# Performance work log

Measured on AMD Instinct MI355X. Metric: run time of the kernel, lower is better.

Reference implementation:

```python
import jax, jax.numpy as jnp
import numpy as np

EMBED_DIM = 1024
NUM_HEADS = 16
HEAD_DIM = EMBED_DIM // NUM_HEADS  # 64
GROUP_SIZE = 4                     # 4 values packed per uint8 (2-bit KIVI)
Q_LEVELS = 3.0                     # 2-bit -> codes in [0, 3]
Q_HALF = 1.5                       # symmetric offset


def kivi_fake_quant(k):
    """Per-group 2-bit quantize+dequantize of keys, KIVI-style.
    k: [B, H, S, D] float32. Groups of GROUP_SIZE along D share one fp32 scale
    (mirrors k_cache_packed uint8 codes + k_scales fp32 in the source).
    """
    B, H, S, D = k.shape
    g = k.reshape(B, H, S, D // GROUP_SIZE, GROUP_SIZE)
    max_abs = jnp.max(jnp.abs(g), axis=-1, keepdims=True)        # per-group scale basis
    scale = max_abs / Q_HALF
    safe = jnp.where(scale == 0, 1.0, scale)
    codes = jnp.clip(jnp.round(g / safe + Q_HALF), 0.0, Q_LEVELS)  # uint8 codes (as float)
    deq = (codes - Q_HALF) * scale                                 # dequant
    return deq.reshape(B, H, S, D)


def split_heads(x):
    B, S, E = x.shape
    return x.reshape(B, S, NUM_HEADS, HEAD_DIM).transpose(0, 2, 1, 3)  # [B,H,S,d]


def setup_inputs() -> dict:
    key = jax.random.key(0)
    k1, k2, k3 = jax.random.split(key, 3)
    B, S = 4, 1024
    return {
        "hidden_states": jax.random.normal(k1, (B, S, EMBED_DIM), jnp.float32),
        "attention_mask": jnp.zeros((B, S), jnp.float32),  # additive mask
        "w_attn": jax.random.normal(k2, (EMBED_DIM, 3 * EMBED_DIM), jnp.float32) * 0.02,
        "b_attn": jnp.zeros((3 * EMBED_DIM,), jnp.float32),
        "w_proj": jax.random.normal(k3, (EMBED_DIM, EMBED_DIM), jnp.float32) * 0.02,
        "b_proj": jnp.zeros((EMBED_DIM,), jnp.float32),
    }


def reference(hidden_states, attention_mask, w_attn, b_attn, w_proj, b_proj):
    B, S, E = hidden_states.shape
    qkv = hidden_states @ w_attn + b_attn            # GPT-2 Conv1D: x @ W + b
    q, k, v = jnp.split(qkv, 3, axis=2)
    q, k, v = split_heads(q), split_heads(k), split_heads(v)   # [B,H,S,d]

    k_deq = kivi_fake_quant(k)                       # quantized KV cache (keys)
    # kivi_sycl.batched_attention: q @ dequant(K)^T over full cache_len (== S here)
    scores = jnp.einsum('bhqd,bhkd->bhqk', q, k_deq)
    # source adds 2-D additive mask BEFORE the 1/sqrt(d) scaling
    scores = scores + attention_mask[:, None, None, :]
    attn = jax.nn.softmax(scores / jnp.sqrt(jnp.float32(HEAD_DIM)), axis=-1)

    out = jnp.einsum('bhqk,bhkd->bhqd', attn, v)     # V cache kept fp32
    out = out.transpose(0, 2, 1, 3).reshape(B, S, E)
    return out @ w_proj + b_proj
```

## Files before the change

kernel.cpp:

```cpp
#include <hip/hip_runtime.h>
#include <math.h>

#define S_LEN 1024
#define B_SZ  4
#define E_DIM 1024
#define NH    16
#define HD    64
#define GK    1024

typedef unsigned short u16;
typedef _Float16 f16;
typedef __attribute__((ext_vector_type(8))) _Float16 f16x8;
typedef __attribute__((ext_vector_type(2))) __fp16   hf16x2;
typedef __attribute__((ext_vector_type(4))) float    f32x4;

#define MFMA16(a, b, c) __builtin_amdgcn_mfma_f32_16x16x32_f16(a, b, c, 0, 0, 0)
#define SCALE2 0.18033688011112042f

__device__ __forceinline__ u16 f2h_bits(float f) {
    union { f16 h; u16 u; } c; c.h = (f16)f;
    return c.u;
}
__device__ __forceinline__ unsigned pk2h(float a, float b) {
    return (unsigned)f2h_bits(a) | ((unsigned)f2h_bits(b) << 16);
}
__device__ __forceinline__ unsigned pkrtz2(float a, float b) {
    hf16x2 t = __builtin_amdgcn_cvt_pkrtz(a, b);
    union { hf16x2 v; unsigned u; } c; c.v = t; return c.u;
}

__device__ __forceinline__ void glds16(const u16* g, u16* l) {
    __builtin_amdgcn_global_load_lds(
        (const __attribute__((address_space(1))) unsigned int*)g,
        (__attribute__((address_space(3))) unsigned int*)l, 16, 0, 0);
}

__global__ __launch_bounds__(256) void prep_all(
    const float* __restrict__ hs, u16* __restrict__ Hh,
    const float* __restrict__ w_attn, u16* __restrict__ Wqt,
    const float* __restrict__ w_proj, u16* __restrict__ Wpt,
    const float* __restrict__ mask, float* __restrict__ Msc)
{
    __shared__ float t[32][33];
    const int bid = blockIdx.x;

    if (bid == 8192) {
        const int i = threadIdx.x * 16;
        #pragma unroll
        for (int k = 0; k < 4; ++k) {
            float4 v = *(const float4*)&mask[i + 4 * k];
            float4 o = { v.x * SCALE2, v.y * SCALE2, v.z * SCALE2, v.w * SCALE2 };
            *(float4*)&Msc[i + 4 * k] = o;
        }
        return;
    }
    if (bid < 4096) {
        const size_t i = ((size_t)bid * 256 + threadIdx.x) * 4;
        float4 v = *(const float4*)&hs[i];
        ushort4 h;
        h.x = f2h_bits(v.x); h.y = f2h_bits(v.y);
        h.z = f2h_bits(v.z); h.w = f2h_bits(v.w);
        *(ushort4*)&Hh[i] = h;
        return;
    }

    const bool isA = bid < 7168;
    const int tt = isA ? (bid - 4096) : (bid - 7168);
    const int bxx = isA ? (tt % 96) : (tt % 32);
    const int byy = isA ? (tt / 96) : (tt / 32);
    const int N   = isA ? 3072 : 1024;
    const float* W = isA ? w_attn : w_proj;
    u16* Wt = isA ? Wqt : Wpt;

    const int k0 = byy * 32, n0 = bxx * 32;
    {
        const int kr = threadIdx.x >> 3, nc = (threadIdx.x & 7) << 2;
        float4 v = *(const float4*)&W[(size_t)(k0 + kr) * N + n0 + nc];
        t[kr][nc] = v.x; t[kr][nc + 1] = v.y; t[kr][nc + 2] = v.z; t[kr][nc + 3] = v.w;
    }
    __syncthreads();
    const int nr = threadIdx.x >> 3, kc = (threadIdx.x & 7) << 2;
    ushort4 h;
    h.x = f2h_bits(t[kc + 0][nr]); h.y = f2h_bits(t[kc + 1][nr]);
    h.z = f2h_bits(t[kc + 2][nr]); h.w = f2h_bits(t[kc + 3][nr]);
    *(ushort4*)&Wt[(size_t)(n0 + nr) * GK + k0 + kc] = h;
}

__global__ __launch_bounds__(256, 4) void qkv_gemm(
    const u16* __restrict__ A, const u16* __restrict__ Bt,
    const float* __restrict__ bias, u16* __restrict__ Qh,
    u16* __restrict__ Kh, u16* __restrict__ Vtg)
{
    __shared__ u16 SLDS[16896];
    u16* Asp = SLDS;
    u16* Bsp = SLDS + 8192;

    const int tid = threadIdx.x;
    const int wave = tid >> 6, lane = tid & 63;
    const int quad = lane >> 4, l15 = lane & 15;
    const int wr = wave >> 1, wc = wave & 1;

    const int m0   = blockIdx.y * 128;
    const int nloc = blockIdx.x * 128;
    const int region = nloc >> 10;

    const u16* Ab = A  + (size_t)m0 * GK;
    const u16* Bb = Bt + (size_t)nloc * GK;

    const int soff = (((lane & 7) ^ ((lane >> 3) & 7)) << 3);
    const int srow8 = lane >> 3;
    const int sw = l15 & 7;

    f32x4 acc[4][4] = {};

    for (int k0 = 0; k0 < GK; k0 += 64) {
        __syncthreads();
        #pragma unroll
        for (int i = 0; i < 4; ++i) {
            const int tI = wave * 4 + i;
            const int row = tI * 8 + srow8;
            glds16(Ab + (size_t)row * GK + k0 + soff, &Asp[tI * 512]);
            glds16(Bb + (size_t)row * GK + k0 + soff, &Bsp[tI * 512]);
        }
        __syncthreads();
        #pragma unroll
        for (int h = 0; h < 2; ++h) {
            const int cs = ((4 * h + quad) ^ sw) << 3;
            f16x8 af[4], bf[4];
            #pragma unroll
            for (int i = 0; i < 4; ++i)
                af[i] = *(const f16x8*)&Asp[(64 * wr + 16 * i + l15) * 64 + cs];
            #pragma unroll
            for (int j = 0; j < 4; ++j)
                bf[j] = *(const f16x8*)&Bsp[(64 * wc + 16 * j + l15) * 64 + cs];
            #pragma unroll
            for (int i = 0; i < 4; ++i)
                #pragma unroll
                for (int j = 0; j < 4; ++j)
                    acc[i][j] = MFMA16(af[i], bf[j], acc[i][j]);
        }
    }

    if (region == 2) {
        #pragma unroll
        for (int j = 0; j < 4; ++j) {
            const int colg = nloc + 64 * wc + 16 * j + l15;
            const float bv = bias[colg];
            const int cr = colg & 1023, h = cr >> 6, d = cr & 63;
            #pragma unroll
            for (int i = 0; i < 4; ++i) {
                const int rowb = m0 + 64 * wr + 16 * i + quad * 4;
                const int b = rowb >> 10, s0 = rowb & 1023;
                float v0 = acc[i][j][0] + bv, v1 = acc[i][j][1] + bv;
                float v2 = acc[i][j][2] + bv, v3 = acc[i][j][3] + bv;
                uint2 st = { pk2h(v0, v1), pk2h(v2, v3) };
                *(uint2*)&Vtg[((size_t)(b * NH + h) * HD + d) * S_LEN + s0] = st;
            }
        }
    } else {
        float* EP = (float*)SLDS;
        u16* dstg = (region == 1) ? Kh : Qh;
        #pragma unroll
        for (int p = 0; p < 2; ++p) {
            __syncthreads();
            if (wr == p) {
                #pragma unroll
                for (int i = 0; i < 4; ++i)
                    #pragma unroll
                    for (int j = 0; j < 4; ++j) {
                        const int colb = 64 * wc + 16 * j + l15;
                        const float bv = bias[nloc + colb];
                        #pragma unroll
                        for (int r = 0; r < 4; ++r)
                            EP[(16 * i + quad * 4 + r) * 132 + colb] = acc[i][j][r] + bv;
                    }
            }
            __syncthreads();
            const int rr = tid >> 2, cc = (tid & 3) * 32;
            const int rowg = m0 + 64 * p + rr;
            const int bb = rowg >> 10, ss = rowg & 1023;
            float v[32];
            #pragma unroll
            for (int k = 0; k < 8; ++k) {
                f32x4 t4 = *(const f32x4*)&EP[rr * 132 + cc + 4 * k];
                v[4 * k + 0] = t4[0]; v[4 * k + 1] = t4[1];
                v[4 * k + 2] = t4[2]; v[4 * k + 3] = t4[3];
            }
            if (region == 1) {
                #pragma unroll
                for (int g = 0; g < 8; ++g) {
                    float a = fmaxf(fmaxf(fabsf(v[4 * g]), fabsf(v[4 * g + 1])),
                                    fmaxf(fabsf(v[4 * g + 2]), fabsf(v[4 * g + 3])));
                    float scale = a * (1.0f / 1.5f);
                    float safe  = (scale == 0.0f) ? 1.0f : scale;
                    #pragma unroll
                    for (int r = 0; r < 4; ++r) {
                        float q = fminf(fmaxf(rintf(v[4 * g + r] / safe + 1.5f), 0.0f), 3.0f);
                        v[4 * g + r] = (q - 1.5f) * scale;
                    }
                }
            }
            unsigned w[16];
            #pragma unroll
            for (int m = 0; m < 16; ++m) w[m] = pk2h(v[2 * m], v[2 * m + 1]);
            const int hh = ((nloc & 1023) + cc) >> 6;
            const int d0 = cc & 63;
            u16* dp = dstg + (((size_t)(bb * NH + hh)) * S_LEN + ss) * HD + d0;
            #pragma unroll
            for (int q4 = 0; q4 < 4; ++q4) {
                uint4 st = { w[4 * q4], w[4 * q4 + 1], w[4 * q4 + 2], w[4 * q4 + 3] };
                *(uint4*)&dp[q4 * 8] = st;
            }
        }
    }
}

__global__ __launch_bounds__(256, 4) void proj_gemm(
    const u16* __restrict__ A, const u16* __restrict__ Bt,
    const float* __restrict__ bias, float* __restrict__ C)
{
    __shared__ u16 Asp[64 * 64];
    __shared__ u16 Bsp[64 * 64];

    const int tid = threadIdx.x;
    const int wave = tid >> 6, lane = tid & 63;
    const int quad = lane >> 4, l15 = lane & 15;
    const int wr = wave >> 1, wc = wave & 1;

    const int m0   = blockIdx.y * 64;
    const int nloc = blockIdx.x * 64;

    const u16* Ab = A  + (size_t)m0 * GK;
    const u16* Bb = Bt + (size_t)nloc * GK;

    const int soff = (((lane & 7) ^ ((lane >> 3) & 7)) << 3);
    const int srow8 = lane >> 3;
    const int sw = l15 & 7;

    f32x4 acc[2][2] = {};

    for (int k0 = 0; k0 < GK; k0 += 64) {
        __syncthreads();
        #pragma unroll
        for (int i = 0; i < 2; ++i) {
            const int tI = wave * 2 + i;
            glds16(Ab + (size_t)(tI * 8 + srow8) * GK + k0 + soff, &Asp[tI * 512]);
            glds16(Bb + (size_t)(tI * 8 + srow8) * GK + k0 + soff, &Bsp[tI * 512]);
        }
        __syncthreads();
        #pragma unroll
        for (int h = 0; h < 2; ++h) {
            const int cs = ((4 * h + quad) ^ sw) << 3;
            f16x8 af[2], bf[2];
            #pragma unroll
            for (int i = 0; i < 2; ++i)
                af[i] = *(const f16x8*)&Asp[(32 * wr + 16 * i + l15) * 64 + cs];
            #pragma unroll
            for (int j = 0; j < 2; ++j)
                bf[j] = *(const f16x8*)&Bsp[(32 * wc + 16 * j + l15) * 64 + cs];
            #pragma unroll
            for (int i = 0; i < 2; ++i)
                #pragma unroll
                for (int j = 0; j < 2; ++j)
                    acc[i][j] = MFMA16(af[i], bf[j], acc[i][j]);
        }
    }

    #pragma unroll
    for (int j = 0; j < 2; ++j) {
        const int col = nloc + 32 * wc + 16 * j + l15;
        const float bv = bias[col];
        #pragma unroll
        for (int i = 0; i < 2; ++i) {
            const int row = m0 + 32 * wr + 16 * i + quad * 4;
            #pragma unroll
            for (int r = 0; r < 4; ++r)
                C[(size_t)(row + r) * E_DIM + col] = acc[i][j][r] + bv;
        }
    }
}

__global__ __launch_bounds__(512, 4) void attn_mfma(
    const u16* __restrict__ Qh, const u16* __restrict__ Kh,
    const u16* __restrict__ Vtg, const float* __restrict__ Msc,
    u16* __restrict__ out)
{
    __shared__ u16 Ks[2][64 * 64];
    __shared__ u16 Vt[2][64 * 64];
    __shared__ u16 Ps[8][16 * 72];
    __shared__ float MsL[1024];

    const int tid  = threadIdx.x;
    const int wave = tid >> 6, lane = tid & 63;
    const int quad = lane >> 4, l15 = lane & 15;

    const int d = blockIdx.x;
    const int j = d >> 3;
    const int head = (d & 7) * 8 + (j & 7);
    const int qt   = j >> 3;
    const int b = head >> 4, h = head & 15;
    const size_t head_base = (size_t)head * (S_LEN * HD);

    if (tid < 256) {
        float4 mv = *(const float4*)&Msc[b * S_LEN + tid * 4];
        *(float4*)&MsL[tid * 4] = mv;
    }

    const int qbase = qt * 128 + wave * 16;
    f16x8 qf0, qf1;
    {
        const u16* qp = Qh + head_base + (size_t)(qbase + l15) * HD + quad * 8;
        qf0 = *(const f16x8*)qp;
        qf1 = *(const f16x8*)(qp + 32);
    }

    f32x4 O[4] = {};
    f32x4 ps_acc = {0.f, 0.f, 0.f, 0.f};

    const u16* Kb = Kh  + head_base;
    const u16* Vb = Vtg + head_base;

    const int srow_ = wave * 8 + (lane >> 3);
    const int skoff = (((lane & 7) ^ ((lane >> 3) & 7)) << 3);
    const int ch0 = ((quad ^ (l15 & 7)) << 3);
    const int ch1 = (((4 + quad) ^ (l15 & 7)) << 3);

    glds16(Kb + (size_t)srow_ * HD + skoff,    &Ks[0][wave * 512]);
    glds16(Vb + (size_t)srow_ * S_LEN + skoff, &Vt[0][wave * 512]);
    __syncthreads();

    for (int kt = 0; kt < 16; ++kt) {
        const int cur = kt & 1;

        if (kt < 15) {
            glds16(Kb + (size_t)((kt + 1) * 64 + srow_) * HD + skoff,
                   &Ks[cur ^ 1][wave * 512]);
            glds16(Vb + (size_t)srow_ * S_LEN + (kt + 1) * 64 + skoff,
                   &Vt[cur ^ 1][wave * 512]);
        }

        const u16* Kl = Ks[cur];
        const u16* Vl = Vt[cur];

        f32x4 acc[4] = {};
        __builtin_amdgcn_s_setprio(1);
        #pragma unroll
        for (int i = 0; i < 4; ++i) {
            const u16* kr = &Kl[(16 * i + l15) * 64];
            acc[i] = MFMA16(*(const f16x8*)&kr[ch0], qf0, acc[i]);
            acc[i] = MFMA16(*(const f16x8*)&kr[ch1], qf1, acc[i]);
        }
        __builtin_amdgcn_s_setprio(0);

        const float* mrow = &MsL[kt * 64];
        f32x4 p4[4];
        #pragma unroll
        for (int i = 0; i < 4; ++i) {
            f32x4 mk = *(const f32x4*)(mrow + 16 * i + quad * 4);
            f32x4 s = acc[i] * SCALE2 + mk;
            p4[i][0] = __builtin_amdgcn_exp2f(s[0]);
            p4[i][1] = __builtin_amdgcn_exp2f(s[1]);
            p4[i][2] = __builtin_amdgcn_exp2f(s[2]);
            p4[i][3] = __builtin_amdgcn_exp2f(s[3]);
            ps_acc += p4[i];
        }

        {
            u16* pw = &Ps[wave][l15 * 72];
            #pragma unroll
            for (int i = 0; i < 4; ++i) {
                *(unsigned*)&pw[16 * i + quad * 4]     = pkrtz2(p4[i][0], p4[i][1]);
                *(unsigned*)&pw[16 * i + quad * 4 + 2] = pkrtz2(p4[i][2], p4[i][3]);
            }
        }

        __builtin_amdgcn_s_setprio(1);
        #pragma unroll
        for (int kc = 0; kc < 2; ++kc) {
            f16x8 pa = *(const f16x8*)&Ps[wave][l15 * 72 + kc * 32 + quad * 8];
            const int chv = kc ? ch1 : ch0;
            #pragma unroll
            for (int i = 0; i < 4; ++i)
                O[i] = MFMA16(pa, *(const f16x8*)&Vl[(16 * i + l15) * 64 + chv], O[i]);
        }
        __builtin_amdgcn_s_setprio(0);

        __syncthreads();
    }

    float psum = (ps_acc[0] + ps_acc[1]) + (ps_acc[2] + ps_acc[3]);
    psum += __shfl_xor(psum, 16);
    psum += __shfl_xor(psum, 32);
    float li[4];
    #pragma unroll
    for (int r = 0; r < 4; ++r) li[r] = 1.0f / __shfl(psum, quad * 4 + r);
    #pragma unroll
    for (int r = 0; r < 4; ++r) {
        u16* orow = out + ((size_t)(b * S_LEN) + qbase + quad * 4 + r) * E_DIM
                    + h * HD + l15;
        orow[0]  = f2h_bits(O[0][r] * li[r]);
        orow[16] = f2h_bits(O[1][r] * li[r]);
        orow[32] = f2h_bits(O[2][r] * li[r]);
        orow[48] = f2h_bits(O[3][r] * li[r]);
    }
}

extern "C" void kernel_launch(void* const* d_in, const int* in_sizes, int n_in,
                              void* d_out, int out_size, void* d_ws, size_t ws_size,
                              hipStream_t stream)
{
    const float* hs     = (const float*)d_in[0];
    const float* mask   = (const float*)d_in[1];
    const float* w_attn = (const float*)d_in[2];
    const float* b_attn = (const float*)d_in[3];
    const float* w_proj = (const float*)d_in[4];
    const float* b_proj = (const float*)d_in[5];
    float* out = (float*)d_out;

    const size_t M1 = (size_t)4096 * 1024;
    u16* Ah   = (u16*)d_ws;
    u16* Wqt  = Ah   + M1;
    u16* Wpt  = Wqt  + 3 * M1;
    u16* Qh   = Wpt  + M1;
    u16* Kh   = Qh   + M1;
    u16* Vtg  = Kh   + M1;
    u16* AOh  = Vtg  + M1;
    float* Msc = (float*)(AOh + M1);

    prep_all<<<8193, 256, 0, stream>>>(hs, Ah, w_attn, Wqt, w_proj, Wpt, mask, Msc);

    qkv_gemm<<<dim3(24, 32), 256, 0, stream>>>(Ah, Wqt, b_attn, Qh, Kh, Vtg);

    attn_mfma<<<B_SZ * NH * (S_LEN / 128), 512, 0, stream>>>(Qh, Kh, Vtg, Msc, AOh);

    proj_gemm<<<dim3(16, 64), 256, 0, stream>>>(AOh, Wpt, b_proj, out);
}
```

Before: 168.5 us.

## Split attention key range across two wave groups per block with LDS merge

Each block now handles 64 query rows instead of 128, with two groups of four waves each covering half the key sequence (split-K). The partial outputs and row sums are merged through shared memory at the end, and the grid doubles to 1024 blocks. Double buffering is replaced by per-group single buffers with two syncs per tile, and the mask is read straight from global memory instead of being staged in LDS. The aim is more blocks and higher occupancy (launch bounds raised to 8), traded against lost load/compute overlap, twice as many Q and K/V loads per query, and the extra merge step.

```diff
diff --git a/kernel.cpp b/kernel.cpp
--- a/kernel.cpp
+++ b/kernel.cpp
@@ -280,33 +280,28 @@
     }
 }
 
-__global__ __launch_bounds__(512, 4) void attn_mfma(
+__global__ __launch_bounds__(512, 8) void attn_mfma(
     const u16* __restrict__ Qh, const u16* __restrict__ Kh,
     const u16* __restrict__ Vtg, const float* __restrict__ Msc,
     u16* __restrict__ out)
 {
     __shared__ u16 Ks[2][64 * 64];
     __shared__ u16 Vt[2][64 * 64];
-    __shared__ u16 Ps[8][16 * 72];
-    __shared__ float MsL[1024];
+    __shared__ u16 Ps[8][16 * 32];
 
     const int tid  = threadIdx.x;
     const int wave = tid >> 6, lane = tid & 63;
     const int quad = lane >> 4, l15 = lane & 15;
+    const int gw = wave & 3;
+    const int g  = wave >> 2;
 
     const int d = blockIdx.x;
-    const int j = d >> 3;
-    const int head = (d & 7) * 8 + (j & 7);
-    const int qt   = j >> 3;
+    const int head = (d & 7) * 8 + ((d >> 3) & 7);
+    const int qt   = d >> 6;
     const int b = head >> 4, h = head & 15;
     const size_t head_base = (size_t)head * (S_LEN * HD);
 
-    if (tid < 256) {
-        float4 mv = *(const float4*)&Msc[b * S_LEN + tid * 4];
-        *(float4*)&MsL[tid * 4] = mv;
-    }
-
-    const int qbase = qt * 128 + wave * 16;
+    const int qbase = qt * 64 + gw * 16;
     f16x8 qf0, qf1;
     {
         const u16* qp = Qh + head_base + (size_t)(qbase + l15) * HD + quad * 8;
@@ -320,75 +315,91 @@
     const u16* Kb = Kh  + head_base;
     const u16* Vb = Vtg + head_base;
 
-    const int srow_ = wave * 8 + (lane >> 3);
+    const int srow  = gw * 16 + (lane >> 3);
     const int skoff = (((lane & 7) ^ ((lane >> 3) & 7)) << 3);
     const int ch0 = ((quad ^ (l15 & 7)) << 3);
     const int ch1 = (((4 + quad) ^ (l15 & 7)) << 3);
 
-    glds16(Kb + (size_t)srow_ * HD + skoff,    &Ks[0][wave * 512]);
-    glds16(Vb + (size_t)srow_ * S_LEN + skoff, &Vt[0][wave * 512]);
-    __syncthreads();
-
-    for (int kt = 0; kt < 16; ++kt) {
-        const int cur = kt & 1;
-
-        if (kt < 15) {
-            glds16(Kb + (size_t)((kt + 1) * 64 + srow_) * HD + skoff,
-                   &Ks[cur ^ 1][wave * 512]);
-            glds16(Vb + (size_t)srow_ * S_LEN + (kt + 1) * 64 + skoff,
-                   &Vt[cur ^ 1][wave * 512]);
-        }
-
-        const u16* Kl = Ks[cur];
-        const u16* Vl = Vt[cur];
+    u16* KsG = Ks[g];
+    u16* VtG = Vt[g];
+    const float* mbase = Msc + b * S_LEN + g * 512;
+
+    for (int t = 0; t < 8; ++t) {
+        const int kt = g * 8 + t;
+        __syncthreads();
+        #pragma unroll
+        for (int p = 0; p < 2; ++p) {
+            glds16(Kb + (size_t)(kt * 64 + srow + p * 8) * HD + skoff,
+                   &KsG[(gw * 16 + p * 8) * 64]);
+            glds16(Vb + (size_t)(srow + p * 8) * S_LEN + kt * 64 + skoff,
+                   &VtG[(gw * 16 + p * 8) * 64]);
+        }
+        __syncthreads();
 
         f32x4 acc[4] = {};
         __builtin_amdgcn_s_setprio(1);
         #pragma unroll
         for (int i = 0; i < 4; ++i) {
-            const u16* kr = &Kl[(16 * i + l15) * 64];
+            const u16* kr = &KsG[(16 * i + l15) * 64];
             acc[i] = MFMA16(*(const f16x8*)&kr[ch0], qf0, acc[i]);
             acc[i] = MFMA16(*(const f16x8*)&kr[ch1], qf1, acc[i]);
         }
         __builtin_amdgcn_s_setprio(0);
 
-        const float* mrow = &MsL[kt * 64];
-        f32x4 p4[4];
+        const float* mrow = mbase + t * 64;
         #pragma unroll
         for (int i = 0; i < 4; ++i) {
             f32x4 mk = *(const f32x4*)(mrow + 16 * i + quad * 4);
             f32x4 s = acc[i] * SCALE2 + mk;
-            p4[i][0] = __builtin_amdgcn_exp2f(s[0]);
-            p4[i][1] = __builtin_amdgcn_exp2f(s[1]);
-            p4[i][2] = __builtin_amdgcn_exp2f(s[2]);
-            p4[i][3] = __builtin_amdgcn_exp2f(s[3]);
-            ps_acc += p4[i];
-        }
-
-        {
-            u16* pw = &Ps[wave][l15 * 72];
-            #pragma unroll
-            for (int i = 0; i < 4; ++i) {
-                *(unsigned*)&pw[16 * i + quad * 4]     = pkrtz2(p4[i][0], p4[i][1]);
-                *(unsigned*)&pw[16 * i + quad * 4 + 2] = pkrtz2(p4[i][2], p4[i][3]);
-            }
-        }
-
+            acc[i][0] = __builtin_amdgcn_exp2f(s[0]);
+            acc[i][1] = __builtin_amdgcn_exp2f(s[1]);
+            acc[i][2] = __builtin_amdgcn_exp2f(s[2]);
+            acc[i][3] = __builtin_amdgcn_exp2f(s[3]);
+            ps_acc += acc[i];
+        }
+
+        u16* pw = &Ps[wave][l15 * 32];
         __builtin_amdgcn_s_setprio(1);
         #pragma unroll
         for (int kc = 0; kc < 2; ++kc) {
-            f16x8 pa = *(const f16x8*)&Ps[wave][l15 * 72 + kc * 32 + quad * 8];
+            #pragma unroll
+            for (int ii = 0; ii < 2; ++ii) {
+                const int i = 2 * kc + ii;
+                *(unsigned*)&pw[16 * ii + quad * 4]     = pkrtz2(acc[i][0], acc[i][1]);
+                *(unsigned*)&pw[16 * ii + quad * 4 + 2] = pkrtz2(acc[i][2], acc[i][3]);
+            }
+            f16x8 pa = *(const f16x8*)&pw[quad * 8];
             const int chv = kc ? ch1 : ch0;
             #pragma unroll
             for (int i = 0; i < 4; ++i)
-                O[i] = MFMA16(pa, *(const f16x8*)&Vl[(16 * i + l15) * 64 + chv], O[i]);
+                O[i] = MFMA16(pa, *(const f16x8*)&VtG[(16 * i + l15) * 64 + chv], O[i]);
         }
         __builtin_amdgcn_s_setprio(0);
-
-        __syncthreads();
-    }
+    }
+
+    __syncthreads();
+    float* SC = (float*)Ks;
+    if (g == 1) {
+        float* p = SC + (gw * 64 + lane) * 21;
+        #pragma unroll
+        for (int i = 0; i < 4; ++i)
+            #pragma unroll
+            for (int r = 0; r < 4; ++r) p[4 * i + r] = O[i][r];
+        p[16] = (ps_acc[0] + ps_acc[1]) + (ps_acc[2] + ps_acc[3]);
+    }
+    __syncthreads();
+    if (g == 1) return;
 
     float psum = (ps_acc[0] + ps_acc[1]) + (ps_acc[2] + ps_acc[3]);
+    {
+        const float* p = SC + (gw * 64 + lane) * 21;
+        #pragma unroll
+        for (int i = 0; i < 4; ++i)
+            #pragma unroll
+            for (int r = 0; r < 4; ++r) O[i][r] += p[4 * i + r];
+        psum += p[16];
+    }
+
     psum += __shfl_xor(psum, 16);
     psum += __shfl_xor(psum, 32);
     float li[4];
@@ -431,7 +442,7 @@
 
     qkv_gemm<<<dim3(24, 32), 256, 0, stream>>>(Ah, Wqt, b_attn, Qh, Kh, Vtg);
 
-    attn_mfma<<<B_SZ * NH * (S_LEN / 128), 512, 0, stream>>>(Qh, Kh, Vtg, Msc, AOh);
+    attn_mfma<<<1024, 512, 0, stream>>>(Qh, Kh, Vtg, Msc, AOh);
 
     proj_gemm<<<dim3(16, 64), 256, 0, stream>>>(AOh, Wpt, b_proj, out);
 }
```

New measurement: 203.1 us. +20.5%, slower.

## Double-buffer QKV GEMM LDS tiles with K=32 steps and MFMA priority boost

Applied to the files above, without the earlier changes.

The QKV GEMM main loop now uses two LDS buffers with a K-step of 32 instead of a single 64-wide buffer. The next tile's global-to-LDS loads are issued before the current tile's MFMAs, and only one barrier remains per iteration. The swizzle is reworked for the 32-wide rows, and s_setprio is raised around the MFMA block. This is meant to overlap memory latency with compute, at the cost of twice as many loop iterations and barriers over K.

```diff
diff --git a/kernel.cpp b/kernel.cpp
--- a/kernel.cpp
+++ b/kernel.cpp
@@ -92,8 +92,6 @@
     u16* __restrict__ Kh, u16* __restrict__ Vtg)
 {
     __shared__ u16 SLDS[16896];
-    u16* Asp = SLDS;
-    u16* Bsp = SLDS + 8192;
 
     const int tid = threadIdx.x;
     const int wave = tid >> 6, lane = tid & 63;
@@ -107,38 +105,54 @@
     const u16* Ab = A  + (size_t)m0 * GK;
     const u16* Bb = Bt + (size_t)nloc * GK;
 
-    const int soff = (((lane & 7) ^ ((lane >> 3) & 7)) << 3);
-    const int srow8 = lane >> 3;
-    const int sw = l15 & 7;
+    const int r16 = lane >> 2;
+    const int sg  = (((lane & 3) ^ ((r16 >> 1) & 3)) << 3);
+    const int rk  = ((quad ^ ((l15 >> 1) & 3)) << 3);
 
     f32x4 acc[4][4] = {};
 
-    for (int k0 = 0; k0 < GK; k0 += 64) {
+    #pragma unroll
+    for (int i = 0; i < 2; ++i) {
+        const int tI = wave * 2 + i;
+        glds16(Ab + (size_t)(tI * 16 + r16) * GK + sg,        SLDS + tI * 512);
+        glds16(Bb + (size_t)(tI * 16 + r16) * GK + sg, SLDS + 8192 + tI * 512);
+    }
+    __syncthreads();
+
+    for (int kt = 0; kt < 32; ++kt) {
+        const int cur = kt & 1;
+        u16* As = SLDS + cur * 4096;
+        u16* Bs = SLDS + 8192 + cur * 4096;
+
+        if (kt < 31) {
+            u16* An = SLDS + (cur ^ 1) * 4096;
+            u16* Bn = SLDS + 8192 + (cur ^ 1) * 4096;
+            const int k1 = (kt + 1) * 32;
+            #pragma unroll
+            for (int i = 0; i < 2; ++i) {
+                const int tI = wave * 2 + i;
+                glds16(Ab + (size_t)(tI * 16 + r16) * GK + k1 + sg, An + tI * 512);
+                glds16(Bb + (size_t)(tI * 16 + r16) * GK + k1 + sg, Bn + tI * 512);
+            }
+        }
+
+        f16x8 af[4], bf[4];
+        #pragma unroll
+        for (int i = 0; i < 4; ++i)
+            af[i] = *(const f16x8*)&As[(64 * wr + 16 * i + l15) * 32 + rk];
+        #pragma unroll
+        for (int j = 0; j < 4; ++j)
+            bf[j] = *(const f16x8*)&Bs[(64 * wc + 16 * j + l15) * 32 + rk];
+
+        __builtin_amdgcn_s_setprio(1);
+        #pragma unroll
+        for (int i = 0; i < 4; ++i)
+            #pragma unroll
+            for (int j = 0; j < 4; ++j)
+                acc[i][j] = MFMA16(af[i], bf[j], acc[i][j]);
+        __builtin_amdgcn_s_setprio(0);
+
         __syncthreads();
-        #pragma unroll
-        for (int i = 0; i < 4; ++i) {
-            const int tI = wave * 4 + i;
-            const int row = tI * 8 + srow8;
-            glds16(Ab + (size_t)row * GK + k0 + soff, &Asp[tI * 512]);
-            glds16(Bb + (size_t)row * GK + k0 + soff, &Bsp[tI * 512]);
-        }
-        __syncthreads();
-        #pragma unroll
-        for (int h = 0; h < 2; ++h) {
-            const int cs = ((4 * h + quad) ^ sw) << 3;
-            f16x8 af[4], bf[4];
-            #pragma unroll
-            for (int i = 0; i < 4; ++i)
-                af[i] = *(const f16x8*)&Asp[(64 * wr + 16 * i + l15) * 64 + cs];
-            #pragma unroll
-            for (int j = 0; j < 4; ++j)
-                bf[j] = *(const f16x8*)&Bsp[(64 * wc + 16 * j + l15) * 64 + cs];
-            #pragma unroll
-            for (int i = 0; i < 4; ++i)
-                #pragma unroll
-                for (int j = 0; j < 4; ++j)
-                    acc[i][j] = MFMA16(af[i], bf[j], acc[i][j]);
-        }
     }
 
     if (region == 2) {
```

New measurement: 167.4 us. Within noise of the previous version (-0.6%).

## Enlarge QKV GEMM tiles to 256x256 with double-buffered LDS prefetch

Applied to the files above, without the earlier changes.

The QKV GEMM moves from 128x128 tiles with 256 threads to 256x256 tiles with 512 threads, a double-buffered LDS pipeline that prefetches the next K-slice while computing the current one, and raised wave priority around the MFMA bursts. The epilogue is restructured into chunked passes through a shared staging buffer so the K quantization and Q/K/V layout writes still fit. This aims to raise arithmetic intensity and overlap global loads with MFMA work. In exchange the grid shrinks to 192 blocks, which may underfill the 256 CUs, and register and LDS use per block grows.

```diff
diff --git a/kernel.cpp b/kernel.cpp
--- a/kernel.cpp
+++ b/kernel.cpp
@@ -86,59 +86,73 @@
     *(ushort4*)&Wt[(size_t)(n0 + nr) * GK + k0 + kc] = h;
 }
 
-__global__ __launch_bounds__(256, 4) void qkv_gemm(
+__global__ __launch_bounds__(512, 2) void qkv_gemm(
     const u16* __restrict__ A, const u16* __restrict__ Bt,
     const float* __restrict__ bias, u16* __restrict__ Qh,
     u16* __restrict__ Kh, u16* __restrict__ Vtg)
 {
-    __shared__ u16 SLDS[16896];
-    u16* Asp = SLDS;
-    u16* Bsp = SLDS + 8192;
+    __shared__ u16 SLDS[65536];
 
     const int tid = threadIdx.x;
     const int wave = tid >> 6, lane = tid & 63;
     const int quad = lane >> 4, l15 = lane & 15;
-    const int wr = wave >> 1, wc = wave & 1;
-
-    const int m0   = blockIdx.y * 128;
-    const int nloc = blockIdx.x * 128;
+    const int wr = wave >> 2, wc = wave & 3;
+
+    const int m0   = blockIdx.y * 256;
+    const int nloc = blockIdx.x * 256;
     const int region = nloc >> 10;
 
     const u16* Ab = A  + (size_t)m0 * GK;
     const u16* Bb = Bt + (size_t)nloc * GK;
 
-    const int soff = (((lane & 7) ^ ((lane >> 3) & 7)) << 3);
     const int srow8 = lane >> 3;
-    const int sw = l15 & 7;
-
-    f32x4 acc[4][4] = {};
-
-    for (int k0 = 0; k0 < GK; k0 += 64) {
-        __syncthreads();
-        #pragma unroll
-        for (int i = 0; i < 4; ++i) {
-            const int tI = wave * 4 + i;
-            const int row = tI * 8 + srow8;
-            glds16(Ab + (size_t)row * GK + k0 + soff, &Asp[tI * 512]);
-            glds16(Bb + (size_t)row * GK + k0 + soff, &Bsp[tI * 512]);
-        }
-        __syncthreads();
-        #pragma unroll
-        for (int h = 0; h < 2; ++h) {
-            const int cs = ((4 * h + quad) ^ sw) << 3;
-            f16x8 af[4], bf[4];
-            #pragma unroll
-            for (int i = 0; i < 4; ++i)
-                af[i] = *(const f16x8*)&Asp[(64 * wr + 16 * i + l15) * 64 + cs];
+    const int soff  = (((lane & 7) ^ (srow8 & 7)) << 3);
+    const int sw    = l15 & 7;
+
+    f32x4 acc[8][4] = {};
+
+    auto STAGE = [&](int kt, int bsel) {
+        u16* Ad = SLDS + bsel * 16384;
+        u16* Bd = SLDS + 32768 + bsel * 16384;
+        const int k0 = kt * 64;
+        #pragma unroll
+        for (int r = 0; r < 4; ++r) {
+            const int g = wave * 4 + r;
+            const int row = g * 8 + srow8;
+            glds16(Ab + (size_t)row * GK + k0 + soff, Ad + g * 512);
+            glds16(Bb + (size_t)row * GK + k0 + soff, Bd + g * 512);
+        }
+    };
+
+    STAGE(0, 0);
+    __syncthreads();
+
+    for (int kt = 0; kt < 16; ++kt) {
+        const int cur = kt & 1;
+        if (kt < 15) STAGE(kt + 1, cur ^ 1);
+
+        const u16* As = SLDS + cur * 16384;
+        const u16* Bs = SLDS + 32768 + cur * 16384;
+
+        #pragma unroll
+        for (int kh = 0; kh < 2; ++kh) {
+            const int cs = ((4 * kh + quad) ^ sw) << 3;
+            f16x8 af[8], bf[4];
+            #pragma unroll
+            for (int i = 0; i < 8; ++i)
+                af[i] = *(const f16x8*)&As[(128 * wr + 16 * i + l15) * 64 + cs];
             #pragma unroll
             for (int j = 0; j < 4; ++j)
-                bf[j] = *(const f16x8*)&Bsp[(64 * wc + 16 * j + l15) * 64 + cs];
-            #pragma unroll
-            for (int i = 0; i < 4; ++i)
+                bf[j] = *(const f16x8*)&Bs[(64 * wc + 16 * j + l15) * 64 + cs];
+            __builtin_amdgcn_s_setprio(1);
+            #pragma unroll
+            for (int i = 0; i < 8; ++i)
                 #pragma unroll
                 for (int j = 0; j < 4; ++j)
                     acc[i][j] = MFMA16(af[i], bf[j], acc[i][j]);
-        }
+            __builtin_amdgcn_s_setprio(0);
+        }
+        __syncthreads();
     }
 
     if (region == 2) {
@@ -148,8 +162,8 @@
             const float bv = bias[colg];
             const int cr = colg & 1023, h = cr >> 6, d = cr & 63;
             #pragma unroll
-            for (int i = 0; i < 4; ++i) {
-                const int rowb = m0 + 64 * wr + 16 * i + quad * 4;
+            for (int i = 0; i < 8; ++i) {
+                const int rowb = m0 + 128 * wr + 16 * i + quad * 4;
                 const int b = rowb >> 10, s0 = rowb & 1023;
                 float v0 = acc[i][j][0] + bv, v1 = acc[i][j][1] + bv;
                 float v2 = acc[i][j][2] + bv, v3 = acc[i][j][3] + bv;
@@ -160,56 +174,67 @@
     } else {
         float* EP = (float*)SLDS;
         u16* dstg = (region == 1) ? Kh : Qh;
-        #pragma unroll
-        for (int p = 0; p < 2; ++p) {
-            __syncthreads();
-            if (wr == p) {
-                #pragma unroll
-                for (int i = 0; i < 4; ++i)
+        for (int p = 0; p < 4; ++p) {
+            for (int ch = 0; ch < 2; ++ch) {
+                __syncthreads();
+                if (wr == (p >> 1) && (wc >> 1) == ch) {
+                    const int wcl = wc & 1;
                     #pragma unroll
-                    for (int j = 0; j < 4; ++j) {
-                        const int colb = 64 * wc + 16 * j + l15;
-                        const float bv = bias[nloc + colb];
+                    for (int ii = 0; ii < 4; ++ii) {
+                        const int i = 4 * (p & 1) + ii;
                         #pragma unroll
-                        for (int r = 0; r < 4; ++r)
-                            EP[(16 * i + quad * 4 + r) * 132 + colb] = acc[i][j][r] + bv;
-                    }
-            }
-            __syncthreads();
-            const int rr = tid >> 2, cc = (tid & 3) * 32;
-            const int rowg = m0 + 64 * p + rr;
-            const int bb = rowg >> 10, ss = rowg & 1023;
-            float v[32];
-            #pragma unroll
-            for (int k = 0; k < 8; ++k) {
-                f32x4 t4 = *(const f32x4*)&EP[rr * 132 + cc + 4 * k];
-                v[4 * k + 0] = t4[0]; v[4 * k + 1] = t4[1];
-                v[4 * k + 2] = t4[2]; v[4 * k + 3] = t4[3];
-            }
-            if (region == 1) {
-                #pragma unroll
-                for (int g = 0; g < 8; ++g) {
-                    float a = fmaxf(fmaxf(fabsf(v[4 * g]), fabsf(v[4 * g + 1])),
-                                    fmaxf(fabsf(v[4 * g + 2]), fabsf(v[4 * g + 3])));
-                    float scale = a * (1.0f / 1.5f);
-                    float safe  = (scale == 0.0f) ? 1.0f : scale;
-                    #pragma unroll
-                    for (int r = 0; r < 4; ++r) {
-                        float q = fminf(fmaxf(rintf(v[4 * g + r] / safe + 1.5f), 0.0f), 3.0f);
-                        v[4 * g + r] = (q - 1.5f) * scale;
+                        for (int j = 0; j < 4; ++j) {
+                            const int colb = 64 * wcl + 16 * j + l15;
+                            const float bv = bias[nloc + 128 * ch + colb];
+                            #pragma unroll
+                            for (int r = 0; r < 4; ++r)
+                                EP[(16 * ii + quad * 4 + r) * 132 + colb] =
+                                    acc[i][j][r] + bv;
+                        }
                     }
                 }
-            }
-            unsigned w[16];
-            #pragma unroll
-            for (int m = 0; m < 16; ++m) w[m] = pk2h(v[2 * m], v[2 * m + 1]);
-            const int hh = ((nloc & 1023) + cc) >> 6;
-            const int d0 = cc & 63;
-            u16* dp = dstg + (((size_t)(bb * NH + hh)) * S_LEN + ss) * HD + d0;
-            #pragma unroll
-            for (int q4 = 0; q4 < 4; ++q4) {
-                uint4 st = { w[4 * q4], w[4 * q4 + 1], w[4 * q4 + 2], w[4 * q4 + 3] };
-                *(uint4*)&dp[q4 * 8] = st;
+                __syncthreads();
+                if (tid < 256) {
+                    const int rr = tid >> 2, cc = (tid & 3) * 32;
+                    const int rowg = m0 + 64 * p + rr;
+                    const int bb = rowg >> 10, ss = rowg & 1023;
+                    float v[32];
+                    #pragma unroll
+                    for (int k = 0; k < 8; ++k) {
+                        f32x4 t4 = *(const f32x4*)&EP[rr * 132 + cc + 4 * k];
+                        v[4 * k + 0] = t4[0]; v[4 * k + 1] = t4[1];
+                        v[4 * k + 2] = t4[2]; v[4 * k + 3] = t4[3];
+                    }
+                    if (region == 1) {
+                        #pragma unroll
+                        for (int g = 0; g < 8; ++g) {
+                            float a = fmaxf(
+                                fmaxf(fabsf(v[4 * g]), fabsf(v[4 * g + 1])),
+                                fmaxf(fabsf(v[4 * g + 2]), fabsf(v[4 * g + 3])));
+                            float scale = a * (1.0f / 1.5f);
+                            float safe  = (scale == 0.0f) ? 1.0f : scale;
+                            #pragma unroll
+                            for (int r = 0; r < 4; ++r) {
+                                float q = fminf(fmaxf(
+                                    rintf(v[4 * g + r] / safe + 1.5f), 0.0f), 3.0f);
+                                v[4 * g + r] = (q - 1.5f) * scale;
+                            }
+                        }
+                    }
+                    unsigned w[16];
+                    #pragma unroll
+                    for (int m = 0; m < 16; ++m)
+                        w[m] = pk2h(v[2 * m], v[2 * m + 1]);
+                    const int hh = ((nloc & 1023) + 128 * ch + cc) >> 6;
+                    const int d0 = cc & 63;
+                    u16* dp = dstg + (((size_t)(bb * NH + hh)) * S_LEN + ss) * HD + d0;
+                    #pragma unroll
+                    for (int q4 = 0; q4 < 4; ++q4) {
+                        uint4 st = { w[4 * q4], w[4 * q4 + 1],
+                                     w[4 * q4 + 2], w[4 * q4 + 3] };
+                        *(uint4*)&dp[q4 * 8] = st;
+                    }
+                }
             }
         }
     }
@@ -429,7 +454,7 @@
 
     prep_all<<<8193, 256, 0, stream>>>(hs, Ah, w_attn, Wqt, w_proj, Wpt, mask, Msc);
 
-    qkv_gemm<<<dim3(24, 32), 256, 0, stream>>>(Ah, Wqt, b_attn, Qh, Kh, Vtg);
+    qkv_gemm<<<dim3(12, 16), 512, 0, stream>>>(Ah, Wqt, b_attn, Qh, Kh, Vtg);
 
     attn_mfma<<<B_SZ * NH * (S_LEN / 128), 512, 0, stream>>>(Qh, Kh, Vtg, Msc, AOh);
 
```

Measured after the change: 644.5 us. +282.6%, slower.
